# Optimization experiments

Hardware: AMD Instinct MI355X
Metric: run time of the kernel (lower is better)

## Reference

```python
import jax, jax.numpy as jnp
import numpy as np

T, B, D, H = 1024, 128, 512, 256

def _linear_params(k, out_dim, in_dim):
    kw, kb = jax.random.split(k)
    s = 1.0 / np.sqrt(in_dim)
    w = jax.random.uniform(kw, (out_dim, in_dim), minval=-s, maxval=s, dtype=jnp.float32)
    b = jax.random.uniform(kb, (out_dim,), minval=-s, maxval=s, dtype=jnp.float32)
    return w, b

def setup_inputs() -> dict:
    key = jax.random.key(0)
    ks = jax.random.split(key, 9)
    x = jax.random.normal(ks[0], (T, B, D), dtype=jnp.float32)
    fc_w, fc_b = _linear_params(ks[1], H, D)
    forget_w, forget_b = _linear_params(ks[2], H, 2 * H)
    input_w, input_b = _linear_params(ks[3], H, 2 * H)
    update_w, update_b = _linear_params(ks[4], H, 2 * H)
    output_w, output_b = _linear_params(ks[5], H, 2 * H)
    cls_w0, cls_b0 = _linear_params(ks[6], H, H)
    cls_w1, cls_b1 = _linear_params(ks[7], H, H)
    cls_w2, cls_b2 = _linear_params(ks[8], 2, H)
    return dict(x=x, fc_w=fc_w, fc_b=fc_b,
                forget_w=forget_w, forget_b=forget_b,
                input_w=input_w, input_b=input_b,
                update_w=update_w, update_b=update_b,
                output_w=output_w, output_b=output_b,
                cls_w0=cls_w0, cls_b0=cls_b0,
                cls_w1=cls_w1, cls_b1=cls_b1,
                cls_w2=cls_w2, cls_b2=cls_b2)

def reference(x, fc_w, fc_b, forget_w, forget_b, input_w, input_b,
              update_w, update_b, output_w, output_b,
              cls_w0, cls_b0, cls_w1, cls_b1, cls_w2, cls_b2):
    # FC + tanh: [T,B,D] -> [T,B,H]
    h = jnp.tanh(x @ fc_w.T + fc_b)

    # LSTM-style gating over the leading time axis (state is [B,H])
    def step(carry, inp):
        hx, cx = carry
        comb = jnp.concatenate([inp, hx], axis=-1)  # [B, 2H]
        f = jax.nn.sigmoid(comb @ forget_w.T + forget_b)
        i = jax.nn.sigmoid(comb @ input_w.T + input_b)
        g = jnp.tanh(comb @ update_w.T + update_b)
        o = jax.nn.sigmoid(comb @ output_w.T + output_b)
        cx = f * cx + i * g
        hx = o * jnp.tanh(cx)
        return (hx, cx), hx

    init = (jnp.zeros((B, H), h.dtype), jnp.zeros((B, H), h.dtype))
    _, hs = jax.lax.scan(step, init, h)  # hs: [T,B,H]

    # classifier MLP (depth=2) -> 2 logits
    z = jax.nn.relu(hs @ cls_w0.T + cls_b0)
    z = jax.nn.relu(z @ cls_w1.T + cls_b1)
    return z @ cls_w2.T + cls_b2  # [T,B,2]
```

## Files before the change

### kernel.cpp

```cpp
#include <hip/hip_runtime.h>
#include <cstdint>

#define TT 1024
#define BB 128
#define DD 512
#define HH 256
#define TBR (TT*BB)

typedef __attribute__((ext_vector_type(8))) short  s8v;
typedef __attribute__((ext_vector_type(4))) float  f4v;
typedef __attribute__((ext_vector_type(4))) unsigned u4v;

__device__ __forceinline__ float sigf(float x) {
    return __builtin_amdgcn_rcpf(1.0f + __expf(-x));
}
__device__ __forceinline__ float tanh_fast(float x) {
    float e = __expf(fabsf(x) * 2.0f);
    float t = 1.0f - 2.0f * __builtin_amdgcn_rcpf(e + 1.0f);
    return copysignf(t, x);
}

__device__ __forceinline__ unsigned rnbf(float f) {
    unsigned u = __builtin_bit_cast(unsigned, f);
    return (u + 0x7FFFu + ((u >> 16) & 1u)) >> 16;
}

__global__ __launch_bounds__(256) void pack_kernel(
    const float* __restrict__ fw, const float* __restrict__ iw,
    const float* __restrict__ uw, const float* __restrict__ ow,
    const float* __restrict__ fb, const float* __restrict__ ib,
    const float* __restrict__ ub, const float* __restrict__ obb,
    float* __restrict__ wx_p, float* __restrict__ wh_p, float* __restrict__ b_p)
{
    const int r = blockIdx.x;
    const int gate = r >> 8, h = r & 255;
    const float* wsrc = gate == 0 ? fw : gate == 1 ? iw : gate == 2 ? uw : ow;
    const float* bsrc = gate == 0 ? fb : gate == 1 ? ib : gate == 2 ? ub : obb;
    const int k = threadIdx.x;
    wx_p[(size_t)r * 256 + k] = wsrc[(size_t)h * 512 + k];
    wh_p[(size_t)r * 256 + k] = wsrc[(size_t)h * 512 + 256 + k];
    if (k == 0) b_p[r] = bsrc[h];
}

__global__ __launch_bounds__(256) void pack_mfma(
    const float* __restrict__ fw, const float* __restrict__ iw,
    const float* __restrict__ uw, const float* __restrict__ ow,
    const float* __restrict__ fb, const float* __restrict__ ib,
    const float* __restrict__ ub, const float* __restrict__ obb,
    float* __restrict__ wx_p, float* __restrict__ wh_p, float* __restrict__ b_p)
{
    const int r = blockIdx.x;
    const int gate = (r >> 5) & 3;
    const int h = (r >> 7) * 32 + (r & 31);
    const float* wsrc = gate == 0 ? fw : gate == 1 ? iw : gate == 2 ? uw : ow;
    const float* bsrc = gate == 0 ? fb : gate == 1 ? ib : gate == 2 ? ub : obb;
    const int k = threadIdx.x;
    wx_p[(size_t)r * 256 + k] = wsrc[(size_t)h * 512 + k];
    wh_p[(size_t)r * 256 + k] = wsrc[(size_t)h * 512 + 256 + k];
    if (k == 0) b_p[r] = bsrc[h];
}

template<int K, int ACT, int PERM>
__global__ __launch_bounds__(256) void gemm_kernel(
    const float* A, const float* __restrict__ W,
    const float* __restrict__ bias, float* C, int N)
{
    __shared__ __align__(16) float As[16][192];
    __shared__ __align__(16) float Wt[16][192];
    const int tid = threadIdx.x;
    const int m0 = blockIdx.x * 128, n0 = blockIdx.y * 128;
    const int tm = tid >> 4, tn = tid & 15;
    const int am = tm * 12, wn = tn * 12;
    float acc[8][8] = {};
    for (int kc = 0; kc < K; kc += 16) {
        #pragma unroll
        for (int i = 0; i < 2; ++i) {
            int f4 = tid + 256 * i;
            int r = f4 >> 2, k4 = (f4 & 3) * 4;
            float4 av = *(const float4*)&A[(size_t)(m0 + r) * K + kc + k4];
            float4 wv = *(const float4*)&W[(size_t)(n0 + r) * K + kc + k4];
            int fo = (r >> 3) * 12 + (r & 7);
            As[k4 + 0][fo] = av.x; As[k4 + 1][fo] = av.y;
            As[k4 + 2][fo] = av.z; As[k4 + 3][fo] = av.w;
            Wt[k4 + 0][fo] = wv.x; Wt[k4 + 1][fo] = wv.y;
            Wt[k4 + 2][fo] = wv.z; Wt[k4 + 3][fo] = wv.w;
        }
        __syncthreads();
        #pragma unroll
        for (int kk = 0; kk < 16; ++kk) {
            float a[8], w[8];
            *(float4*)&a[0] = *(const float4*)&As[kk][am];
            *(float4*)&a[4] = *(const float4*)&As[kk][am + 4];
            *(float4*)&w[0] = *(const float4*)&Wt[kk][wn];
            *(float4*)&w[4] = *(const float4*)&Wt[kk][wn + 4];
            #pragma unroll
            for (int i = 0; i < 8; ++i)
                #pragma unroll
                for (int j = 0; j < 8; ++j)
                    acc[i][j] = fmaf(a[i], w[j], acc[i][j]);
        }
        __syncthreads();
    }
    #pragma unroll
    for (int i = 0; i < 8; ++i) {
        int m = m0 + tm * 8 + i;
        #pragma unroll
        for (int jh = 0; jh < 2; ++jh) {
            float4 v; float* vp = (float*)&v;
            #pragma unroll
            for (int l = 0; l < 4; ++l) {
                int n = n0 + tn * 8 + jh * 4 + l;
                float t = acc[i][jh * 4 + l] + bias[n];
                if (ACT == 1) t = tanhf(t);
                if (ACT == 2) t = fmaxf(t, 0.0f);
                vp[l] = t;
            }
            int nb = n0 + tn * 8 + jh * 4;
            int nc = PERM ? (((nb & 255) >> 3) * 32 + ((nb >> 8) << 3) + (nb & 7)) : nb;
            *(float4*)&C[(size_t)m * N + nc] = v;
        }
    }
}

__global__ __launch_bounds__(256, 1) void recur_mfma(
    float* __restrict__ h_buf,
    const float* __restrict__ hfc,
    const float* __restrict__ wx_mf,
    const float* __restrict__ wh_mf,
    const float* __restrict__ b_mf,
    unsigned long long* __restrict__ ring)
{
    __shared__ __align__(16) unsigned ldsH[16 * 128];
    __shared__ __align__(16) unsigned ldsL[16 * 128];
    __shared__ __align__(16) unsigned ldsXH[16 * 128];
    __shared__ __align__(16) unsigned ldsXL[16 * 128];
    __shared__ float pre[16][132];
    const int tid = threadIdx.x;
    const int lane = tid & 63;
    const int wv = tid >> 6;
    const int bg = blockIdx.x & 7, hg = blockIdx.x >> 3;
    const int b0 = bg * 16;
    const int nlo = lane & 15, quad = lane >> 4;

    s8v bh[2][8], bl[2][8];
    s8v ch[2][8], cl[2][8];
#define PACK_FRAGS(SRCPTR, BH, BL)                                            \
    _Pragma("unroll")                                                         \
    for (int nt = 0; nt < 2; ++nt) {                                          \
        int r = hg * 128 + wv * 32 + nt * 16 + nlo;                           \
        _Pragma("unroll")                                                     \
        for (int ks = 0; ks < 8; ++ks) {                                      \
            const float* src = SRCPTR + (size_t)r * 256 + ks * 32 + quad * 8; \
            u4v uh, ul;                                                       \
            _Pragma("unroll")                                                 \
            for (int p = 0; p < 4; ++p) {                                     \
                float f0 = src[2 * p], f1 = src[2 * p + 1];                   \
                unsigned h0 = rnbf(f0), h1 = rnbf(f1);                        \
                float r0 = f0 - __builtin_bit_cast(float, h0 << 16);          \
                float r1 = f1 - __builtin_bit_cast(float, h1 << 16);          \
                uh[p] = h0 | (h1 << 16);                                      \
                ul[p] = rnbf(r0) | (rnbf(r1) << 16);                          \
            }                                                                 \
            BH[nt][ks] = __builtin_bit_cast(s8v, uh);                         \
            BL[nt][ks] = __builtin_bit_cast(s8v, ul);                         \
        }                                                                     \
    }
    PACK_FRAGS(wh_mf, bh, bl)
    PACK_FRAGS(wx_mf, ch, cl)
#undef PACK_FRAGS

    const int sm = tid >> 4;
    const int sc0 = (tid & 15) * 2;
    const int cb = tid >> 4, q = tid & 15;
    const unsigned long long SENT = ~0ull;

    float bsf[4][2];
    #pragma unroll
    for (int g = 0; g < 4; ++g) {
        bsf[g][0] = b_mf[hg * 128 + g * 32 + 2 * q];
        bsf[g][1] = b_mf[hg * 128 + g * 32 + 2 * q + 1];
    }

    const int p0 = sm * 128 + ((sc0 ^ (sm & 7)) << 2);
    const int p1 = sm * 128 + (((sc0 + 1) ^ (sm & 7)) << 2);

    float4 xf[4];
    {
        const float* xr = hfc + ((size_t)0 * BB + b0 + sm) * 256 + (tid & 15) * 16;
        xf[0] = *(const float4*)&xr[0];
        xf[1] = *(const float4*)&xr[4];
        xf[2] = *(const float4*)&xr[8];
        xf[3] = *(const float4*)&xr[12];
    }

    float cx0 = 0.0f, cx1 = 0.0f;

    for (int t = 0; t < TT; ++t) {
        {
            const float* fv = (const float*)xf;
            u4v xh0, xl0, xh1, xl1;
            #pragma unroll
            for (int p = 0; p < 4; ++p) {
                float f0 = fv[2 * p], f1 = fv[2 * p + 1];
                unsigned h0 = rnbf(f0), h1 = rnbf(f1);
                xh0[p] = h0 | (h1 << 16);
                xl0[p] = rnbf(f0 - __builtin_bit_cast(float, h0 << 16)) |
                         (rnbf(f1 - __builtin_bit_cast(float, h1 << 16)) << 16);
                float g0 = fv[8 + 2 * p], g1 = fv[8 + 2 * p + 1];
                unsigned k0 = rnbf(g0), k1 = rnbf(g1);
                xh1[p] = k0 | (k1 << 16);
                xl1[p] = rnbf(g0 - __builtin_bit_cast(float, k0 << 16)) |
                         (rnbf(g1 - __builtin_bit_cast(float, k1 << 16)) << 16);
            }
            *(u4v*)&ldsXH[p0] = xh0; *(u4v*)&ldsXH[p1] = xh1;
            *(u4v*)&ldsXL[p0] = xl0; *(u4v*)&ldsXL[p1] = xl1;
        }
        __syncthreads();

        f4v acc0 = {0.f, 0.f, 0.f, 0.f}, acc1 = {0.f, 0.f, 0.f, 0.f};
        #pragma unroll
        for (int ks = 0; ks < 8; ++ks) {
            int off = nlo * 128 + ((((ks * 4 + quad) ^ (nlo & 7))) << 2);
            s8v ah = __builtin_bit_cast(s8v, *(const u4v*)&ldsXH[off]);
            s8v al = __builtin_bit_cast(s8v, *(const u4v*)&ldsXL[off]);
            acc0 = __builtin_amdgcn_mfma_f32_16x16x32_bf16(ah, ch[0][ks], acc0, 0, 0, 0);
            acc1 = __builtin_amdgcn_mfma_f32_16x16x32_bf16(ah, ch[1][ks], acc1, 0, 0, 0);
            acc0 = __builtin_amdgcn_mfma_f32_16x16x32_bf16(al, ch[0][ks], acc0, 0, 0, 0);
            acc1 = __builtin_amdgcn_mfma_f32_16x16x32_bf16(al, ch[1][ks], acc1, 0, 0, 0);
            acc0 = __builtin_amdgcn_mfma_f32_16x16x32_bf16(ah, cl[0][ks], acc0, 0, 0, 0);
            acc1 = __builtin_amdgcn_mfma_f32_16x16x32_bf16(ah, cl[1][ks], acc1, 0, 0, 0);
        }

        if (t == 0) {
            u4v z = {0u, 0u, 0u, 0u};
            *(u4v*)&ldsH[p0] = z; *(u4v*)&ldsH[p1] = z;
            *(u4v*)&ldsL[p0] = z; *(u4v*)&ldsL[p1] = z;
        } else {
            unsigned long long* src =
                ring + ((size_t)((t - 1) & 3) * 128 + b0 + sm) * 128 + sc0 * 4;
            unsigned long long a[8];
            long bud = 1L << 22;
            for (;;) {
                #pragma unroll
                for (int i = 0; i < 8; ++i)
                    a[i] = __hip_atomic_load(&src[i], __ATOMIC_RELAXED,
                                             __HIP_MEMORY_SCOPE_AGENT);
                bool ok = true;
                #pragma unroll
                for (int i = 0; i < 8; ++i) ok = ok && (a[i] != SENT);
                if (__all(ok)) break;
                if (--bud < 0) break;
                __builtin_amdgcn_s_sleep(1);
            }
            u4v w0 = { (unsigned)a[0], (unsigned)a[1], (unsigned)a[2], (unsigned)a[3] };
            u4v w1 = { (unsigned)a[4], (unsigned)a[5], (unsigned)a[6], (unsigned)a[7] };
            u4v v0 = { (unsigned)(a[0] >> 32), (unsigned)(a[1] >> 32),
                       (unsigned)(a[2] >> 32), (unsigned)(a[3] >> 32) };
            u4v v1 = { (unsigned)(a[4] >> 32), (unsigned)(a[5] >> 32),
                       (unsigned)(a[6] >> 32), (unsigned)(a[7] >> 32) };
            *(u4v*)&ldsH[p0] = w0; *(u4v*)&ldsH[p1] = w1;
            *(u4v*)&ldsL[p0] = v0; *(u4v*)&ldsL[p1] = v1;
            if (t >= 2) {
                __hip_atomic_store(
                    &ring[((size_t)((t - 2) & 3) * 128 + b0 + cb) * 128 + hg * 16 + q],
                    SENT, __ATOMIC_RELAXED, __HIP_MEMORY_SCOPE_AGENT);
            }
        }

        {
            int tn2 = (t + 1 < TT) ? (t + 1) : (TT - 1);
            const float* xr = hfc + ((size_t)tn2 * BB + b0 + sm) * 256 + (tid & 15) * 16;
            xf[0] = *(const float4*)&xr[0];
            xf[1] = *(const float4*)&xr[4];
            xf[2] = *(const float4*)&xr[8];
            xf[3] = *(const float4*)&xr[12];
        }
        __syncthreads();

        #pragma unroll
        for (int ks = 0; ks < 8; ++ks) {
            int off = nlo * 128 + ((((ks * 4 + quad) ^ (nlo & 7))) << 2);
            s8v ah = __builtin_bit_cast(s8v, *(const u4v*)&ldsH[off]);
            s8v al = __builtin_bit_cast(s8v, *(const u4v*)&ldsL[off]);
            acc0 = __builtin_amdgcn_mfma_f32_16x16x32_bf16(ah, bh[0][ks], acc0, 0, 0, 0);
            acc1 = __builtin_amdgcn_mfma_f32_16x16x32_bf16(ah, bh[1][ks], acc1, 0, 0, 0);
            acc0 = __builtin_amdgcn_mfma_f32_16x16x32_bf16(al, bh[0][ks], acc0, 0, 0, 0);
            acc1 = __builtin_amdgcn_mfma_f32_16x16x32_bf16(al, bh[1][ks], acc1, 0, 0, 0);
            acc0 = __builtin_amdgcn_mfma_f32_16x16x32_bf16(ah, bl[0][ks], acc0, 0, 0, 0);
            acc1 = __builtin_amdgcn_mfma_f32_16x16x32_bf16(ah, bl[1][ks], acc1, 0, 0, 0);
        }
        {
            int n0c = wv * 32 + nlo;
            #pragma unroll
            for (int reg = 0; reg < 4; ++reg) {
                pre[quad * 4 + reg][n0c]      = acc0[reg];
                pre[quad * 4 + reg][n0c + 16] = acc1[reg];
            }
        }
        __syncthreads();

        float2 pf = *(const float2*)&pre[cb][0 * 32 + 2 * q];
        float2 pi = *(const float2*)&pre[cb][1 * 32 + 2 * q];
        float2 pg = *(const float2*)&pre[cb][2 * 32 + 2 * q];
        float2 po = *(const float2*)&pre[cb][3 * 32 + 2 * q];
        float f0 = sigf(pf.x + bsf[0][0]), f1 = sigf(pf.y + bsf[0][1]);
        float i0 = sigf(pi.x + bsf[1][0]), i1 = sigf(pi.y + bsf[1][1]);
        float g0 = tanh_fast(pg.x + bsf[2][0]), g1 = tanh_fast(pg.y + bsf[2][1]);
        float o0 = sigf(po.x + bsf[3][0]), o1 = sigf(po.y + bsf[3][1]);
        cx0 = f0 * cx0 + i0 * g0;
        cx1 = f1 * cx1 + i1 * g1;
        float hv0 = o0 * tanh_fast(cx0);
        float hv1 = o1 * tanh_fast(cx1);

        unsigned hb0 = rnbf(hv0), hb1 = rnbf(hv1);
        float l0 = hv0 - __builtin_bit_cast(float, hb0 << 16);
        float l1 = hv1 - __builtin_bit_cast(float, hb1 << 16);
        unsigned long long atom =
            (unsigned long long)(hb0 | (hb1 << 16)) |
            ((unsigned long long)(rnbf(l0) | (rnbf(l1) << 16)) << 32);
        __hip_atomic_store(
            &ring[((size_t)(t & 3) * 128 + b0 + cb) * 128 + hg * 16 + q],
            atom, __ATOMIC_RELAXED, __HIP_MEMORY_SCOPE_AGENT);
        *(float2*)&h_buf[((size_t)t * BB + b0 + cb) * 256 + hg * 32 + 2 * q] =
            make_float2(hv0, hv1);
    }
}

__device__ __forceinline__ int swz(int row, int k4) {
    return row * 256 + (((k4 ^ (row & 7)) & 63) << 2);
}

__global__ __launch_bounds__(256, 1) void recur_kernel(
    float* h_buf, const float* __restrict__ xg,
    const float* __restrict__ wx_p, const float* __restrict__ wh_p,
    const float* __restrict__ b_p, float* hx_buf, int* flags, int use_xg)
{
    __shared__ __align__(16) float Ws[32 * 256];
    __shared__ __align__(16) float Ss[32 * 256];
    const int tid = threadIdx.x;
    const int lane = tid & 63;
    const int bg = blockIdx.x & 3, hg = blockIdx.x >> 2;
    const int b0 = bg * 32;
    const int b = tid >> 3, h = tid & 7;
    const int wrow = tid >> 3;
    const int wkb = (tid & 7) * 32;

    float bias0 = b_p[0 * 256 + hg * 8 + h];
    float bias1 = b_p[1 * 256 + hg * 8 + h];
    float bias2 = b_p[2 * 256 + hg * 8 + h];
    float bias3 = b_p[3 * 256 + hg * 8 + h];
    __syncthreads();

    float cx = 0.0f, pv = 0.0f;

    for (int t = 0; t < TT; ++t) {
        if (t > 0) {
            const int* fp = flags + (size_t)(t - 1) * 128 + bg * 32 + (lane & 31);
            long bud = 1L << 22;
            for (;;) {
                int v = __hip_atomic_load(fp, __ATOMIC_RELAXED, __HIP_MEMORY_SCOPE_AGENT);
                if (__all(v != 0)) break;
                if (--bud < 0) break;
                __builtin_amdgcn_s_sleep(1);
            }
        }
        float acc0, acc1, acc2, acc3;
        {
            if (t > 0)
                h_buf[((size_t)(t - 1) * BB + b0 + b) * 256 + hg * 8 + h] = pv;
            acc0 = bias0; acc1 = bias1; acc2 = bias2; acc3 = bias3;
            {
                const int R = (wrow >> 3) * 256 + hg * 8 + (wrow & 7);
                const float* src = wx_p + (size_t)R * 256 + wkb;
                #pragma unroll
                for (int j = 0; j < 8; ++j)
                    *(float4*)&Ws[swz(wrow, (wkb >> 2) + j)] = *(const float4*)&src[j * 4];
                const float* hs = h_buf + ((size_t)t * BB + b0) * HH;
                #pragma unroll
                for (int i = 0; i < 32; ++i)
                    Ss[i * 256 + ((((tid >> 2) ^ (i & 7)) & 63) << 2) + (tid & 3)] =
                        hs[i * 256 + tid];
            }
            __syncthreads();
            #pragma unroll 4
            for (int k4 = 0; k4 < 64; ++k4) {
                float4 s  = *(const float4*)&Ss[swz(b, k4)];
                float4 w0 = *(const float4*)&Ws[(0 * 8 + h) * 256 + (((k4 ^ h) & 63) << 2)];
                float4 w1 = *(const float4*)&Ws[(1 * 8 + h) * 256 + (((k4 ^ h) & 63) << 2)];
                float4 w2 = *(const float4*)&Ws[(2 * 8 + h) * 256 + (((k4 ^ h) & 63) << 2)];
                float4 w3 = *(const float4*)&Ws[(3 * 8 + h) * 256 + (((k4 ^ h) & 63) << 2)];
                acc0 += s.x*w0.x + s.y*w0.y + s.z*w0.z + s.w*w0.w;
                acc1 += s.x*w1.x + s.y*w1.y + s.z*w1.z + s.w*w1.w;
                acc2 += s.x*w2.x + s.y*w2.y + s.z*w2.z + s.w*w2.w;
                acc3 += s.x*w3.x + s.y*w3.y + s.z*w3.z + s.w*w3.w;
            }
            __syncthreads();
            {
                const int R = (wrow >> 3) * 256 + hg * 8 + (wrow & 7);
                const float* src = wh_p + (size_t)R * 256 + wkb;
                #pragma unroll
                for (int j = 0; j < 8; ++j)
                    *(float4*)&Ws[swz(wrow, (wkb >> 2) + j)] = *(const float4*)&src[j * 4];
            }
        }
        {
            const float* hxr = hx_buf + (size_t)(t & 1) * (BB * HH) + (size_t)b0 * HH;
            #pragma unroll
            for (int i = 0; i < 32; ++i) {
                float v = __hip_atomic_load(&hxr[i * 256 + tid],
                                            __ATOMIC_RELAXED, __HIP_MEMORY_SCOPE_AGENT);
                Ss[i * 256 + ((((tid >> 2) ^ (i & 7)) & 63) << 2) + (tid & 3)] = v;
            }
        }
        __syncthreads();
        #pragma unroll 4
        for (int k4 = 0; k4 < 64; ++k4) {
            float4 s  = *(const float4*)&Ss[swz(b, k4)];
            float4 w0 = *(const float4*)&Ws[(0 * 8 + h) * 256 + (((k4 ^ h) & 63) << 2)];
            float4 w1 = *(const float4*)&Ws[(1 * 8 + h) * 256 + (((k4 ^ h) & 63) << 2)];
            float4 w2 = *(const float4*)&Ws[(2 * 8 + h) * 256 + (((k4 ^ h) & 63) << 2)];
            float4 w3 = *(const float4*)&Ws[(3 * 8 + h) * 256 + (((k4 ^ h) & 63) << 2)];
            acc0 += s.x*w0.x + s.y*w0.y + s.z*w0.z + s.w*w0.w;
            acc1 += s.x*w1.x + s.y*w1.y + s.z*w1.z + s.w*w1.w;
            acc2 += s.x*w2.x + s.y*w2.y + s.z*w2.z + s.w*w2.w;
            acc3 += s.x*w3.x + s.y*w3.y + s.z*w3.z + s.w*w3.w;
        }
        __syncthreads();

        float fg = sigf(acc0), ig = sigf(acc1), gg = tanhf(acc2), og = sigf(acc3);
        cx = fg * cx + ig * gg;
        float hxv = og * tanhf(cx);
        pv = hxv;

        __hip_atomic_store(
            &hx_buf[(size_t)((t + 1) & 1) * (BB * HH) + (size_t)(b0 + b) * HH + hg * 8 + h],
            hxv, __ATOMIC_RELAXED, __HIP_MEMORY_SCOPE_AGENT);
        asm volatile("s_waitcnt vmcnt(0)" ::: "memory");
        __syncthreads();
        if (tid == 0)
            __hip_atomic_store(&flags[(size_t)t * 128 + bg * 32 + hg], 1,
                               __ATOMIC_RELAXED, __HIP_MEMORY_SCOPE_AGENT);
    }

    {
        const int* fp = flags + (size_t)1023 * 128 + bg * 32 + (lane & 31);
        long bud = 1L << 22;
        for (;;) {
            int v = __hip_atomic_load(fp, __ATOMIC_RELAXED, __HIP_MEMORY_SCOPE_AGENT);
            if (__all(v != 0)) break;
            if (--bud < 0) break;
            __builtin_amdgcn_s_sleep(1);
        }
        h_buf[((size_t)1023 * BB + b0 + b) * 256 + hg * 8 + h] = pv;
    }
}

__global__ __launch_bounds__(256) void final_kernel(
    const float* __restrict__ z, const float* __restrict__ w2,
    const float* __restrict__ b2, float* __restrict__ out)
{
    const int m = blockIdx.x * 128 + (threadIdx.x >> 1);
    const int c = threadIdx.x & 1;
    const float* zr = z + (size_t)m * 256;
    const float* wr = w2 + (size_t)c * 256;
    float s = b2[c];
    #pragma unroll 8
    for (int k = 0; k < 256; k += 4) {
        float4 zv = *(const float4*)&zr[k];
        float4 wv = *(const float4*)&wr[k];
        s += zv.x*wv.x + zv.y*wv.y + zv.z*wv.z + zv.w*wv.w;
    }
    out[(size_t)m * 2 + c] = s;
}

extern "C" void kernel_launch(void* const* d_in, const int* in_sizes, int n_in,
                              void* d_out, int out_size, void* d_ws, size_t ws_size,
                              hipStream_t stream) {
    const float* x    = (const float*)d_in[0];
    const float* fc_w = (const float*)d_in[1];
    const float* fc_b = (const float*)d_in[2];
    const float* fw   = (const float*)d_in[3];
    const float* fb   = (const float*)d_in[4];
    const float* iw   = (const float*)d_in[5];
    const float* ib   = (const float*)d_in[6];
    const float* uw   = (const float*)d_in[7];
    const float* ub   = (const float*)d_in[8];
    const float* ow   = (const float*)d_in[9];
    const float* ob   = (const float*)d_in[10];
    const float* w0   = (const float*)d_in[11];
    const float* b0   = (const float*)d_in[12];
    const float* w1   = (const float*)d_in[13];
    const float* b1   = (const float*)d_in[14];
    const float* w2   = (const float*)d_in[15];
    const float* b2   = (const float*)d_in[16];
    float* out = (float*)d_out;

    float* ws = (float*)d_ws;
    size_t off = 0;
    float* h_buf  = ws + off; off += (size_t)TBR * HH;
    float* wx_p   = ws + off; off += 1024 * 256;
    float* wh_p   = ws + off; off += 1024 * 256;
    float* b_p    = ws + off; off += 1024;
    float* hx_buf = ws + off; off += 2 * BB * HH;
    float* sync_f = ws + off; off += 131072;
    const size_t base_f = off;
    float* hfc = ws + base_f;
    const size_t need = (base_f + (size_t)TBR * 256) * sizeof(float);
    const int use_mfma = (ws_size >= need) ? 1 : 0;
    float* z0 = ws + base_f;

    if (use_mfma) {
        hipMemsetAsync(sync_f, 0xFF, 131072 * sizeof(float), stream);
        pack_mfma<<<1024, 256, 0, stream>>>(fw, iw, uw, ow, fb, ib, ub, ob,
                                            wx_p, wh_p, b_p);
        gemm_kernel<512, 1, 0><<<dim3(TBR / 128, 2), 256, 0, stream>>>(
            x, fc_w, fc_b, hfc, 256);
        recur_mfma<<<64, 256, 0, stream>>>(h_buf, hfc, wx_p, wh_p, b_p,
                                           (unsigned long long*)sync_f);
    } else {
        hipMemsetAsync(hx_buf, 0, (2 * BB * HH + 131072) * sizeof(float), stream);
        pack_kernel<<<1024, 256, 0, stream>>>(fw, iw, uw, ow, fb, ib, ub, ob,
                                              wx_p, wh_p, b_p);
        gemm_kernel<512, 1, 0><<<dim3(TBR / 128, 2), 256, 0, stream>>>(
            x, fc_w, fc_b, h_buf, 256);
        recur_kernel<<<128, 256, 0, stream>>>(h_buf, nullptr, wx_p, wh_p, b_p,
                                              hx_buf, (int*)sync_f, 0);
    }
    gemm_kernel<256, 2, 0><<<dim3(TBR / 128, 2), 256, 0, stream>>>(
        h_buf, w0, b0, z0, 256);
    gemm_kernel<256, 2, 0><<<dim3(TBR / 128, 2), 256, 0, stream>>>(
        z0, w1, b1, h_buf, 256);
    final_kernel<<<TBR / 128, 256, 0, stream>>>(h_buf, w2, b2, out);
}
```

Before: 4.485 ms.

## Use split-bf16 MFMA GEMMs for FC and classifier, prefetch recurrence ring loads

Replaces the fp32 SIMT GEMMs for the input FC and the two classifier layers with MFMA kernels. These emulate fp32 by splitting activations and pre-packed weights into bf16 hi/lo parts and summing three products. In the recurrent kernel, the ring-buffer atomic loads and the next-step hfc loads are issued before the x-side MFMAs so they overlap compute. Plain syncthreads are swapped for an lgkmcnt wait plus s_barrier. The sync buffer is reused as scratch for the packed weights, which means the memset now has to run after the FC GEMM; the bf16 split also adds a small accuracy risk.

```diff
diff --git a/kernel.cpp b/kernel.cpp
--- a/kernel.cpp
+++ b/kernel.cpp
@@ -24,6 +24,11 @@
     unsigned u = __builtin_bit_cast(unsigned, f);
     return (u + 0x7FFFu + ((u >> 16) & 1u)) >> 16;
 }
+
+#define BAR_LGKM() do { \
+    asm volatile("s_waitcnt lgkmcnt(0)" ::: "memory"); \
+    __builtin_amdgcn_s_barrier(); \
+} while (0)
 
 __global__ __launch_bounds__(256) void pack_kernel(
     const float* __restrict__ fw, const float* __restrict__ iw,
@@ -58,6 +63,20 @@
     wx_p[(size_t)r * 256 + k] = wsrc[(size_t)h * 512 + k];
     wh_p[(size_t)r * 256 + k] = wsrc[(size_t)h * 512 + 256 + k];
     if (k == 0) b_p[r] = bsrc[h];
+}
+
+__global__ __launch_bounds__(256) void pack_wsplit(
+    const float* __restrict__ w, unsigned short* __restrict__ whi,
+    unsigned short* __restrict__ wlo, int K)
+{
+    const int n = blockIdx.x;
+    for (int k = threadIdx.x; k < K; k += 256) {
+        float f = w[(size_t)n * K + k];
+        unsigned h = rnbf(f);
+        float r = f - __builtin_bit_cast(float, h << 16);
+        whi[(size_t)n * K + k] = (unsigned short)h;
+        wlo[(size_t)n * K + k] = (unsigned short)rnbf(r);
+    }
 }
 
 template<int K, int ACT, int PERM>
@@ -118,6 +137,98 @@
             int nb = n0 + tn * 8 + jh * 4;
             int nc = PERM ? (((nb & 255) >> 3) * 32 + ((nb >> 8) << 3) + (nb & 7)) : nb;
             *(float4*)&C[(size_t)m * N + nc] = v;
+        }
+    }
+}
+
+template<int K, int ACT>
+__global__ __launch_bounds__(256) void gemm_bf16s(
+    const float* __restrict__ A, const unsigned short* __restrict__ whi,
+    const unsigned short* __restrict__ wlo, const float* __restrict__ bias,
+    float* __restrict__ C)
+{
+    __shared__ __align__(16) unsigned ldsAH[128 * 16];
+    __shared__ __align__(16) unsigned ldsAL[128 * 16];
+    const int tid = threadIdx.x;
+    const int lane = tid & 63;
+    const int wv = tid >> 6;
+    const int m0 = blockIdx.x * 128;
+    const int n0 = blockIdx.y * 128 + wv * 32;
+    const int nlo = lane & 15, quad = lane >> 4;
+    const int sr = tid >> 1, sg = tid & 1;
+
+    f4v acc[8][2];
+    #pragma unroll
+    for (int i = 0; i < 8; ++i) {
+        acc[i][0] = f4v{0.f, 0.f, 0.f, 0.f};
+        acc[i][1] = f4v{0.f, 0.f, 0.f, 0.f};
+    }
+
+    for (int kc = 0; kc < K; kc += 32) {
+        {
+            const float* ar = A + (size_t)(m0 + sr) * K + kc + sg * 16;
+            float fv[16];
+            *(float4*)&fv[0]  = *(const float4*)&ar[0];
+            *(float4*)&fv[4]  = *(const float4*)&ar[4];
+            *(float4*)&fv[8]  = *(const float4*)&ar[8];
+            *(float4*)&fv[12] = *(const float4*)&ar[12];
+            u4v h0, h1, l0, l1;
+            #pragma unroll
+            for (int p = 0; p < 4; ++p) {
+                float a0 = fv[2 * p], a1 = fv[2 * p + 1];
+                unsigned x0 = rnbf(a0), x1 = rnbf(a1);
+                h0[p] = x0 | (x1 << 16);
+                l0[p] = rnbf(a0 - __builtin_bit_cast(float, x0 << 16)) |
+                        (rnbf(a1 - __builtin_bit_cast(float, x1 << 16)) << 16);
+                float c0 = fv[8 + 2 * p], c1 = fv[8 + 2 * p + 1];
+                unsigned y0 = rnbf(c0), y1 = rnbf(c1);
+                h1[p] = y0 | (y1 << 16);
+                l1[p] = rnbf(c0 - __builtin_bit_cast(float, y0 << 16)) |
+                        (rnbf(c1 - __builtin_bit_cast(float, y1 << 16)) << 16);
+            }
+            int base = sr * 16 + sg * 8;
+            *(u4v*)&ldsAH[base]     = h0; *(u4v*)&ldsAH[base + 4] = h1;
+            *(u4v*)&ldsAL[base]     = l0; *(u4v*)&ldsAL[base + 4] = l1;
+        }
+        __syncthreads();
+
+        s8v bhh[2], bll[2];
+        #pragma unroll
+        for (int nt = 0; nt < 2; ++nt) {
+            size_t roff = (size_t)(n0 + nt * 16 + nlo) * K + kc + quad * 8;
+            bhh[nt] = *(const s8v*)&whi[roff];
+            bll[nt] = *(const s8v*)&wlo[roff];
+        }
+        #pragma unroll
+        for (int mt = 0; mt < 8; ++mt) {
+            int off = (mt * 16 + nlo) * 16 + quad * 4;
+            s8v ah = __builtin_bit_cast(s8v, *(const u4v*)&ldsAH[off]);
+            s8v al = __builtin_bit_cast(s8v, *(const u4v*)&ldsAL[off]);
+            acc[mt][0] = __builtin_amdgcn_mfma_f32_16x16x32_bf16(ah, bhh[0], acc[mt][0], 0, 0, 0);
+            acc[mt][1] = __builtin_amdgcn_mfma_f32_16x16x32_bf16(ah, bhh[1], acc[mt][1], 0, 0, 0);
+            acc[mt][0] = __builtin_amdgcn_mfma_f32_16x16x32_bf16(al, bhh[0], acc[mt][0], 0, 0, 0);
+            acc[mt][1] = __builtin_amdgcn_mfma_f32_16x16x32_bf16(al, bhh[1], acc[mt][1], 0, 0, 0);
+            acc[mt][0] = __builtin_amdgcn_mfma_f32_16x16x32_bf16(ah, bll[0], acc[mt][0], 0, 0, 0);
+            acc[mt][1] = __builtin_amdgcn_mfma_f32_16x16x32_bf16(ah, bll[1], acc[mt][1], 0, 0, 0);
+        }
+        __syncthreads();
+    }
+
+    float bv0 = bias[n0 + nlo];
+    float bv1 = bias[n0 + 16 + nlo];
+    #pragma unroll
+    for (int mt = 0; mt < 8; ++mt) {
+        #pragma unroll
+        for (int nt = 0; nt < 2; ++nt) {
+            float bv = nt ? bv1 : bv0;
+            int n = n0 + nt * 16 + nlo;
+            #pragma unroll
+            for (int reg = 0; reg < 4; ++reg) {
+                float t = acc[mt][nt][reg] + bv;
+                if (ACT == 1) t = tanhf(t);
+                if (ACT == 2) t = fmaxf(t, 0.0f);
+                C[(size_t)(m0 + mt * 16 + quad * 4 + reg) * 256 + n] = t;
+            }
         }
     }
 }
@@ -215,7 +326,26 @@
             *(u4v*)&ldsXH[p0] = xh0; *(u4v*)&ldsXH[p1] = xh1;
             *(u4v*)&ldsXL[p0] = xl0; *(u4v*)&ldsXL[p1] = xl1;
         }
-        __syncthreads();
+        BAR_LGKM();
+
+        unsigned long long pa[8];
+        const unsigned long long* srcp =
+            ring + ((size_t)((t - 1) & 3) * 128 + b0 + sm) * 128 + sc0 * 4;
+        if (t > 0) {
+            #pragma unroll
+            for (int i = 0; i < 8; ++i)
+                pa[i] = __hip_atomic_load(&srcp[i], __ATOMIC_RELAXED,
+                                          __HIP_MEMORY_SCOPE_AGENT);
+        }
+        {
+            int tn2 = (t + 1 < TT) ? (t + 1) : (TT - 1);
+            const float* xr = hfc + ((size_t)tn2 * BB + b0 + sm) * 256 + (tid & 15) * 16;
+            xf[0] = *(const float4*)&xr[0];
+            xf[1] = *(const float4*)&xr[4];
+            xf[2] = *(const float4*)&xr[8];
+            xf[3] = *(const float4*)&xr[12];
+        }
+        __builtin_amdgcn_sched_barrier(0);
 
         f4v acc0 = {0.f, 0.f, 0.f, 0.f}, acc1 = {0.f, 0.f, 0.f, 0.f};
         #pragma unroll
@@ -230,34 +360,37 @@
             acc0 = __builtin_amdgcn_mfma_f32_16x16x32_bf16(ah, cl[0][ks], acc0, 0, 0, 0);
             acc1 = __builtin_amdgcn_mfma_f32_16x16x32_bf16(ah, cl[1][ks], acc1, 0, 0, 0);
         }
+        __builtin_amdgcn_sched_barrier(0);
 
         if (t == 0) {
             u4v z = {0u, 0u, 0u, 0u};
             *(u4v*)&ldsH[p0] = z; *(u4v*)&ldsH[p1] = z;
             *(u4v*)&ldsL[p0] = z; *(u4v*)&ldsL[p1] = z;
         } else {
-            unsigned long long* src =
-                ring + ((size_t)((t - 1) & 3) * 128 + b0 + sm) * 128 + sc0 * 4;
-            unsigned long long a[8];
-            long bud = 1L << 22;
-            for (;;) {
-                #pragma unroll
-                for (int i = 0; i < 8; ++i)
-                    a[i] = __hip_atomic_load(&src[i], __ATOMIC_RELAXED,
-                                             __HIP_MEMORY_SCOPE_AGENT);
-                bool ok = true;
-                #pragma unroll
-                for (int i = 0; i < 8; ++i) ok = ok && (a[i] != SENT);
-                if (__all(ok)) break;
-                if (--bud < 0) break;
-                __builtin_amdgcn_s_sleep(1);
-            }
-            u4v w0 = { (unsigned)a[0], (unsigned)a[1], (unsigned)a[2], (unsigned)a[3] };
-            u4v w1 = { (unsigned)a[4], (unsigned)a[5], (unsigned)a[6], (unsigned)a[7] };
-            u4v v0 = { (unsigned)(a[0] >> 32), (unsigned)(a[1] >> 32),
-                       (unsigned)(a[2] >> 32), (unsigned)(a[3] >> 32) };
-            u4v v1 = { (unsigned)(a[4] >> 32), (unsigned)(a[5] >> 32),
-                       (unsigned)(a[6] >> 32), (unsigned)(a[7] >> 32) };
+            bool ok = true;
+            #pragma unroll
+            for (int i = 0; i < 8; ++i) ok = ok && (pa[i] != SENT);
+            if (!__all(ok)) {
+                long bud = 1L << 22;
+                for (;;) {
+                    #pragma unroll
+                    for (int i = 0; i < 8; ++i)
+                        pa[i] = __hip_atomic_load(&srcp[i], __ATOMIC_RELAXED,
+                                                  __HIP_MEMORY_SCOPE_AGENT);
+                    ok = true;
+                    #pragma unroll
+                    for (int i = 0; i < 8; ++i) ok = ok && (pa[i] != SENT);
+                    if (__all(ok)) break;
+                    if (--bud < 0) break;
+                    __builtin_amdgcn_s_sleep(1);
+                }
+            }
+            u4v w0 = { (unsigned)pa[0], (unsigned)pa[1], (unsigned)pa[2], (unsigned)pa[3] };
+            u4v w1 = { (unsigned)pa[4], (unsigned)pa[5], (unsigned)pa[6], (unsigned)pa[7] };
+            u4v v0 = { (unsigned)(pa[0] >> 32), (unsigned)(pa[1] >> 32),
+                       (unsigned)(pa[2] >> 32), (unsigned)(pa[3] >> 32) };
+            u4v v1 = { (unsigned)(pa[4] >> 32), (unsigned)(pa[5] >> 32),
+                       (unsigned)(pa[6] >> 32), (unsigned)(pa[7] >> 32) };
             *(u4v*)&ldsH[p0] = w0; *(u4v*)&ldsH[p1] = w1;
             *(u4v*)&ldsL[p0] = v0; *(u4v*)&ldsL[p1] = v1;
             if (t >= 2) {
@@ -266,16 +399,7 @@
                     SENT, __ATOMIC_RELAXED, __HIP_MEMORY_SCOPE_AGENT);
             }
         }
-
-        {
-            int tn2 = (t + 1 < TT) ? (t + 1) : (TT - 1);
-            const float* xr = hfc + ((size_t)tn2 * BB + b0 + sm) * 256 + (tid & 15) * 16;
-            xf[0] = *(const float4*)&xr[0];
-            xf[1] = *(const float4*)&xr[4];
-            xf[2] = *(const float4*)&xr[8];
-            xf[3] = *(const float4*)&xr[12];
-        }
-        __syncthreads();
+        BAR_LGKM();
 
         #pragma unroll
         for (int ks = 0; ks < 8; ++ks) {
@@ -297,7 +421,7 @@
                 pre[quad * 4 + reg][n0c + 16] = acc1[reg];
             }
         }
-        __syncthreads();
+        BAR_LGKM();
 
         float2 pf = *(const float2*)&pre[cb][0 * 32 + 2 * q];
         float2 pi = *(const float2*)&pre[cb][1 * 32 + 2 * q];
@@ -510,13 +634,27 @@
     float* z0 = ws + base_f;
 
     if (use_mfma) {
-        hipMemsetAsync(sync_f, 0xFF, 131072 * sizeof(float), stream);
+        unsigned* syncu = (unsigned*)sync_f;
+        unsigned short* fchi = (unsigned short*)syncu;
+        unsigned short* fclo = (unsigned short*)(syncu + 65536);
+        pack_wsplit<<<256, 256, 0, stream>>>(fc_w, fchi, fclo, 512);
         pack_mfma<<<1024, 256, 0, stream>>>(fw, iw, uw, ow, fb, ib, ub, ob,
                                             wx_p, wh_p, b_p);
-        gemm_kernel<512, 1, 0><<<dim3(TBR / 128, 2), 256, 0, stream>>>(
-            x, fc_w, fc_b, hfc, 256);
+        gemm_bf16s<512, 1><<<dim3(TBR / 128, 2), 256, 0, stream>>>(
+            x, fchi, fclo, fc_b, hfc);
+        hipMemsetAsync(sync_f, 0xFF, 131072 * sizeof(float), stream);
         recur_mfma<<<64, 256, 0, stream>>>(h_buf, hfc, wx_p, wh_p, b_p,
                                            (unsigned long long*)sync_f);
+        unsigned short* w0hi = (unsigned short*)syncu;
+        unsigned short* w0lo = (unsigned short*)(syncu + 32768);
+        unsigned short* w1hi = (unsigned short*)(syncu + 65536);
+        unsigned short* w1lo = (unsigned short*)(syncu + 98304);
+        pack_wsplit<<<256, 256, 0, stream>>>(w0, w0hi, w0lo, 256);
+        pack_wsplit<<<256, 256, 0, stream>>>(w1, w1hi, w1lo, 256);
+        gemm_bf16s<256, 2><<<dim3(TBR / 128, 2), 256, 0, stream>>>(
+            h_buf, w0hi, w0lo, b0, z0);
+        gemm_bf16s<256, 2><<<dim3(TBR / 128, 2), 256, 0, stream>>>(
+            z0, w1hi, w1lo, b1, h_buf);
     } else {
         hipMemsetAsync(hx_buf, 0, (2 * BB * HH + 131072) * sizeof(float), stream);
         pack_kernel<<<1024, 256, 0, stream>>>(fw, iw, uw, ow, fb, ib, ub, ob,
@@ -525,10 +663,10 @@
             x, fc_w, fc_b, h_buf, 256);
         recur_kernel<<<128, 256, 0, stream>>>(h_buf, nullptr, wx_p, wh_p, b_p,
                                               hx_buf, (int*)sync_f, 0);
-    }
-    gemm_kernel<256, 2, 0><<<dim3(TBR / 128, 2), 256, 0, stream>>>(
-        h_buf, w0, b0, z0, 256);
-    gemm_kernel<256, 2, 0><<<dim3(TBR / 128, 2), 256, 0, stream>>>(
-        z0, w1, b1, h_buf, 256);
+        gemm_kernel<256, 2, 0><<<dim3(TBR / 128, 2), 256, 0, stream>>>(
+            h_buf, w0, b0, z0, 256);
+        gemm_kernel<256, 2, 0><<<dim3(TBR / 128, 2), 256, 0, stream>>>(
+            z0, w1, b1, h_buf, 256);
+    }
     final_kernel<<<TBR / 128, 256, 0, stream>>>(h_buf, w2, b2, out);
 }
```

New measurement: 4.111 ms. 8.3% less time.
